# Kernel optimization log

Measured on AMD Instinct MI355X. Metric: run time of the kernel, lower is better.

Reference implementation:

```python
import jax, jax.numpy as jnp
import numpy as np

# Stickbreaking attention (IBM ModuleFormer style) as in the torch module:
#   logits = q @ k^T / sqrt(head_dim)  (causal)
#   z = sigmoid(logits), log_beta = logsigmoid(-logits), both causally masked
#   re_cum_log_beta = einsum('bhij,jk->bhik', log_beta, tril(ones(S,S)))
#     -> re[i,k] = sum_{k <= j <= i} log_beta[i, j]   (full tril incl. diagonal,
#        exactly as written in the source: cum_weight = torch.tril(torch.ones(L,L)))
#   weights = z * exp(re_cum_log_beta);  out = weights @ v
# Note: the torch code applies the causal mask by adding -inf; the only finite,
# NaN-free expression of that math (matching ModuleFormer's masked_fill) is to
# zero out masked entries of z and log_beta before the triangular matmul.

B, H, S, D = 2, 16, 1024, 64


def setup_inputs() -> dict:
    key = jax.random.key(0)
    kq, kk, kv = jax.random.split(key, 3)
    q = jax.random.normal(kq, (B, H, S, D), dtype=jnp.float32)
    k = jax.random.normal(kk, (B, H, S, D), dtype=jnp.float32)
    v = jax.random.normal(kv, (B, H, S, D), dtype=jnp.float32)
    return {"q": q, "k": k, "v": v}


def reference(q, k, v):
    head_dim = q.shape[-1]
    scaling = 1.0 / np.sqrt(head_dim).astype(np.float32)
    # [B,H,S,S] attention logits
    logits = jnp.einsum("bhqd,bhkd->bhqk", q, k) * scaling
    seq = logits.shape[-1]
    causal = jnp.tril(jnp.ones((seq, seq), dtype=logits.dtype))  # 1 where j<=i
    z = jax.nn.sigmoid(logits) * causal
    log_beta = jax.nn.log_sigmoid(-logits) * causal
    cum_weight = jnp.tril(jnp.ones((seq, seq), dtype=logits.dtype))
    # re[i,k] = sum_{j>=k} log_beta[i,j] (log_beta already 0 for j>i)
    re_cum_log_beta = jnp.einsum("bhij,jk->bhik", log_beta, cum_weight)
    weights = z * jnp.exp(re_cum_log_beta)
    return jnp.einsum("bhqk,bhkd->bhqd", weights, v)
```

## Files before the change

kernel.cpp:

```cpp
#include <hip/hip_runtime.h>
#include <hip/hip_bf16.h>
#include <math.h>


typedef __attribute__((ext_vector_type(8))) short short8;
typedef __attribute__((ext_vector_type(4))) short short4v;
typedef __attribute__((ext_vector_type(4))) float f32x4;

#define PITCH 72

__device__ inline short bf16r(float x) {
    __hip_bfloat16 h = __float2bfloat16(x);
    return *(short*)&h;
}
__device__ inline float bf16f(short s) {
    union { unsigned u; float f; } c;
    c.u = ((unsigned)(unsigned short)s) << 16;
    return c.f;
}
__device__ inline void tsplit(float x, short &hi, short &lo) {
    union { float f; unsigned u; } c; c.f = x;
    hi = (short)(c.u >> 16);
    union { unsigned u; float f; } h; h.u = c.u & 0xFFFF0000u;
    union { float f; unsigned u; } r; r.f = x - h.f;
    lo = (short)(r.u >> 16);
}

__device__ inline void lds_barrier() {
    __builtin_amdgcn_sched_barrier(0);
    asm volatile("s_waitcnt lgkmcnt(0)" ::: "memory");
    __builtin_amdgcn_s_barrier();
    __builtin_amdgcn_sched_barrier(0);
}

__global__ __launch_bounds__(256, 2) void stickbreak_mfma(
    const float* __restrict__ Qg, const float* __restrict__ Kg,
    const float* __restrict__ Vg, float* __restrict__ Og)
{
    __shared__ __align__(16) short Kh[2][64 * PITCH];
    __shared__ __align__(16) short Kl[2][64 * PITCH];
    __shared__ __align__(16) short Vt[2][64 * PITCH];
    __shared__ __align__(16) short Ws[64 * PITCH];

    const int t = threadIdx.x;
    const int n = blockIdx.x;
    const int bh = (n & 7) + 8 * (n >> 7);
    const int qr = (n >> 3) & 15;
    const int qt = (n >> 8) ? (15 - qr) : qr;

    const size_t hbase = (size_t)bh * 1024 * 64;
    const float* qp = Qg + hbase + (size_t)qt * 64 * 64;
    const float* kp = Kg + hbase;
    const float* vp = Vg + hbase;
    float*       op = Og + hbase + (size_t)qt * 64 * 64;

    const int lane = t & 63;
    const int wv   = t >> 6;
    const int l16  = lane & 15;
    const int q4   = lane >> 4;

    const int srow = t >> 2;
    const int scol = (t & 3) << 4;
    const int vj   = (t & 15) << 2;
    const int vd   = (t >> 4) << 2;

    short8 qfh[2], qfl[2];
    {
        const float* qrow = qp + (16 * wv + l16) * 64;
        #pragma unroll
        for (int ks = 0; ks < 2; ++ks) {
            const int base = 32 * ks + 8 * q4;
            const float4 f0 = *(const float4*)(qrow + base);
            const float4 f1 = *(const float4*)(qrow + base + 4);
            float a[8] = {f0.x, f0.y, f0.z, f0.w, f1.x, f1.y, f1.z, f1.w};
            #pragma unroll
            for (int j = 0; j < 8; ++j) {
                short hi, lo;
                tsplit(a[j], hi, lo);
                qfh[ks][j] = hi;
                qfl[ks][j] = lo;
            }
        }
    }

    f32x4 Oacc[4];
    #pragma unroll
    for (int i = 0; i < 4; ++i) Oacc[i] = (f32x4){0.f, 0.f, 0.f, 0.f};
    float Prow = 1.f;

    float4 kreg[4], vreg[4];

    auto prefetch_tile = [&](int tt) {
        const float* ksrc = kp + (size_t)tt * 4096 + srow * 64 + scol;
        const float* vsrc = vp + (size_t)tt * 4096;
        #pragma unroll
        for (int i = 0; i < 4; ++i) kreg[i] = *(const float4*)(ksrc + 4 * i);
        #pragma unroll
        for (int r = 0; r < 4; ++r) vreg[r] = *(const float4*)(vsrc + (vj + r) * 64 + vd);
    };

    auto stage_tile = [&](int nb) {
        short8 h0, h1, l0, l1;
        #pragma unroll
        for (int i = 0; i < 4; ++i) {
            float a[4] = {kreg[i].x, kreg[i].y, kreg[i].z, kreg[i].w};
            #pragma unroll
            for (int j = 0; j < 4; ++j) {
                short hi, lo;
                tsplit(a[j], hi, lo);
                const int idx = 4 * i + j;
                if (idx < 8) { h0[idx] = hi; l0[idx] = lo; }
                else         { h1[idx - 8] = hi; l1[idx - 8] = lo; }
            }
        }
        *(short8*)&Kh[nb][srow * PITCH + scol]     = h0;
        *(short8*)&Kh[nb][srow * PITCH + scol + 8] = h1;
        *(short8*)&Kl[nb][srow * PITCH + scol]     = l0;
        *(short8*)&Kl[nb][srow * PITCH + scol + 8] = l1;
        #pragma unroll
        for (int x = 0; x < 4; ++x) {
            float rr[4] = { x == 0 ? vreg[0].x : x == 1 ? vreg[0].y : x == 2 ? vreg[0].z : vreg[0].w,
                            x == 0 ? vreg[1].x : x == 1 ? vreg[1].y : x == 2 ? vreg[1].z : vreg[1].w,
                            x == 0 ? vreg[2].x : x == 1 ? vreg[2].y : x == 2 ? vreg[2].z : vreg[2].w,
                            x == 0 ? vreg[3].x : x == 1 ? vreg[3].y : x == 2 ? vreg[3].z : vreg[3].w };
            short4v w4;
            #pragma unroll
            for (int r = 0; r < 4; ++r) w4[r] = bf16r(rr[r]);
            *(short4v*)&Vt[nb][(vd + x) * PITCH + vj] = w4;
        }
    };

    prefetch_tile(qt);
    stage_tile(0);
    if (qt > 0) prefetch_tile(qt - 1);
    lds_barrier();

    for (int kt = qt; kt >= 0; --kt) {
        const int cur = (qt - kt) & 1;

        f32x4 Sacc[4];
        #pragma unroll
        for (int i = 0; i < 4; ++i) Sacc[i] = (f32x4){0.f, 0.f, 0.f, 0.f};
        #pragma unroll
        for (int ks = 0; ks < 2; ++ks) {
            #pragma unroll
            for (int nt = 0; nt < 4; ++nt) {
                const short8 ah = *(const short8*)&Kh[cur][(16 * nt + l16) * PITCH + 32 * ks + 8 * q4];
                const short8 al = *(const short8*)&Kl[cur][(16 * nt + l16) * PITCH + 32 * ks + 8 * q4];
                Sacc[nt] = __builtin_amdgcn_mfma_f32_16x16x32_bf16(ah, qfh[ks], Sacc[nt], 0, 0, 0);
                Sacc[nt] = __builtin_amdgcn_mfma_f32_16x16x32_bf16(al, qfh[ks], Sacc[nt], 0, 0, 0);
                Sacc[nt] = __builtin_amdgcn_mfma_f32_16x16x32_bf16(ah, qfl[ks], Sacc[nt], 0, 0, 0);
            }
        }

        const bool diag = (kt == qt);
        const int irow = 16 * wv + l16;
        const float C = 0.180336880f;
        float zp[4][4];
        float sR[4];
        #pragma unroll
        for (int nt = 0; nt < 4; ++nt) {
            float b[4], zz[4];
            #pragma unroll
            for (int reg = 0; reg < 4; ++reg) {
                float l2 = Sacc[nt][reg] * C;
                if (diag && (16 * nt + 4 * q4 + reg > irow)) l2 = -1e30f;
                l2 = fminf(l2, 80.f);
                const float e  = __builtin_amdgcn_exp2f(l2);
                const float bb = __builtin_amdgcn_rcpf(1.f + e);
                b[reg] = bb;
                zz[reg] = e * bb;
            }
            const float p3 = b[3];
            const float p2 = b[2] * p3;
            const float p1 = b[1] * p2;
            const float p0 = b[0] * p1;
            zp[nt][0] = zz[0] * p0;
            zp[nt][1] = zz[1] * p1;
            zp[nt][2] = zz[2] * p2;
            zp[nt][3] = zz[3] * p3;
            sR[nt] = p0;
        }
        float ex4[4], Tn[4];
        #pragma unroll
        for (int nt = 0; nt < 4; ++nt) {
            float g = sR[nt];
            float u = __shfl_down(g, 16, 64); if (q4 < 3) g *= u;
            u = __shfl_down(g, 32, 64);       if (q4 < 2) g *= u;
            const float x = __shfl_down(g, 16, 64);
            ex4[nt] = (q4 == 3) ? 1.f : x;
            Tn[nt]  = __shfl(g, l16, 64);
        }
        const float TSa[4] = { Tn[1] * Tn[2] * Tn[3], Tn[2] * Tn[3], Tn[3], 1.f };
        #pragma unroll
        for (int nt = 0; nt < 4; ++nt) {
            const float cross = ex4[nt] * TSa[nt] * Prow;
            short4v w4;
            #pragma unroll
            for (int reg = 0; reg < 4; ++reg)
                w4[reg] = bf16r(zp[nt][reg] * cross);
            *(short4v*)&Ws[irow * PITCH + 16 * nt + 4 * q4] = w4;
        }
        Prow *= TSa[0] * Tn[0];

        #pragma unroll
        for (int ks = 0; ks < 2; ++ks) {
            const short8 wa = *(const short8*)&Ws[(16 * wv + l16) * PITCH + 32 * ks + 8 * q4];
            #pragma unroll
            for (int dt = 0; dt < 4; ++dt) {
                const short8 vb = *(const short8*)&Vt[cur][(16 * dt + l16) * PITCH + 32 * ks + 8 * q4];
                Oacc[dt] = __builtin_amdgcn_mfma_f32_16x16x32_bf16(wa, vb, Oacc[dt], 0, 0, 0);
            }
        }

        if (kt > 0) {
            stage_tile(cur ^ 1);
            if (kt > 1) prefetch_tile(kt - 2);
            lds_barrier();
        }
    }

    #pragma unroll
    for (int dt = 0; dt < 4; ++dt)
        #pragma unroll
        for (int r = 0; r < 4; ++r)
            op[(16 * wv + 4 * q4 + r) * 64 + 16 * dt + l16] = Oacc[dt][r];
}

extern "C" void kernel_launch(void* const* d_in, const int* in_sizes, int n_in,
                              void* d_out, int out_size, void* d_ws, size_t ws_size,
                              hipStream_t stream) {
    const float* q = (const float*)d_in[0];
    const float* k = (const float*)d_in[1];
    const float* v = (const float*)d_in[2];
    float* out = (float*)d_out;
    stickbreak_mfma<<<dim3(512), dim3(256), 0, stream>>>(q, k, v, out);
}
```

Before: 96.73 us.

## Permute K tile rows so score accumulators feed PV MFMA directly from registers

K rows are written to shared memory in a permuted order, so the S=K·Q MFMA output lands in registers in exactly the layout the W·V MFMA needs as its A operand. This removes the Ws shared-memory round trip (a store, a reload and the implied ordering) and rewrites the stick-breaking prefix products around the new column ordering, with fewer shuffles. The cost is more intricate index math for the causal mask and the cumulative products, which raises the risk of subtle ordering errors.

```diff
diff --git a/kernel.cpp b/kernel.cpp
--- a/kernel.cpp
+++ b/kernel.cpp
@@ -40,7 +40,6 @@
     __shared__ __align__(16) short Kh[2][64 * PITCH];
     __shared__ __align__(16) short Kl[2][64 * PITCH];
     __shared__ __align__(16) short Vt[2][64 * PITCH];
-    __shared__ __align__(16) short Ws[64 * PITCH];
 
     const int t = threadIdx.x;
     const int n = blockIdx.x;
@@ -61,6 +60,8 @@
 
     const int srow = t >> 2;
     const int scol = (t & 3) << 4;
+    const int kprm = (((srow >> 2) & 1) << 5) | (((srow >> 5) & 1) << 4)
+                   | (((srow >> 3) & 3) << 2) | (srow & 3);
     const int vj   = (t & 15) << 2;
     const int vd   = (t >> 4) << 2;
 
@@ -113,10 +114,10 @@
                 else         { h1[idx - 8] = hi; l1[idx - 8] = lo; }
             }
         }
-        *(short8*)&Kh[nb][srow * PITCH + scol]     = h0;
-        *(short8*)&Kh[nb][srow * PITCH + scol + 8] = h1;
-        *(short8*)&Kl[nb][srow * PITCH + scol]     = l0;
-        *(short8*)&Kl[nb][srow * PITCH + scol + 8] = l1;
+        *(short8*)&Kh[nb][kprm * PITCH + scol]     = h0;
+        *(short8*)&Kh[nb][kprm * PITCH + scol + 8] = h1;
+        *(short8*)&Kl[nb][kprm * PITCH + scol]     = l0;
+        *(short8*)&Kl[nb][kprm * PITCH + scol + 8] = l1;
         #pragma unroll
         for (int x = 0; x < 4; ++x) {
             float rr[4] = { x == 0 ? vreg[0].x : x == 1 ? vreg[0].y : x == 2 ? vreg[0].z : vreg[0].w,
@@ -164,53 +165,56 @@
             #pragma unroll
             for (int reg = 0; reg < 4; ++reg) {
                 float l2 = Sacc[nt][reg] * C;
-                if (diag && (16 * nt + 4 * q4 + reg > irow)) l2 = -1e30f;
+                const int j = 32 * (nt & 1) + 8 * q4 + 4 * (nt >> 1) + reg;
+                if (diag && (j > irow)) l2 = -1e30f;
                 l2 = fminf(l2, 80.f);
                 const float e  = __builtin_amdgcn_exp2f(l2);
                 const float bb = __builtin_amdgcn_rcpf(1.f + e);
                 b[reg] = bb;
                 zz[reg] = e * bb;
             }
-            const float p3 = b[3];
-            const float p2 = b[2] * p3;
-            const float p1 = b[1] * p2;
-            const float p0 = b[0] * p1;
-            zp[nt][0] = zz[0] * p0;
-            zp[nt][1] = zz[1] * p1;
-            zp[nt][2] = zz[2] * p2;
-            zp[nt][3] = zz[3] * p3;
-            sR[nt] = p0;
-        }
-        float ex4[4], Tn[4];
-        #pragma unroll
-        for (int nt = 0; nt < 4; ++nt) {
-            float g = sR[nt];
-            float u = __shfl_down(g, 16, 64); if (q4 < 3) g *= u;
-            u = __shfl_down(g, 32, 64);       if (q4 < 2) g *= u;
-            const float x = __shfl_down(g, 16, 64);
-            ex4[nt] = (q4 == 3) ? 1.f : x;
-            Tn[nt]  = __shfl(g, l16, 64);
-        }
-        const float TSa[4] = { Tn[1] * Tn[2] * Tn[3], Tn[2] * Tn[3], Tn[3], 1.f };
-        #pragma unroll
-        for (int nt = 0; nt < 4; ++nt) {
-            const float cross = ex4[nt] * TSa[nt] * Prow;
-            short4v w4;
-            #pragma unroll
-            for (int reg = 0; reg < 4; ++reg)
-                w4[reg] = bf16r(zp[nt][reg] * cross);
-            *(short4v*)&Ws[irow * PITCH + 16 * nt + 4 * q4] = w4;
-        }
-        Prow *= TSa[0] * Tn[0];
-
-        #pragma unroll
-        for (int ks = 0; ks < 2; ++ks) {
-            const short8 wa = *(const short8*)&Ws[(16 * wv + l16) * PITCH + 32 * ks + 8 * q4];
-            #pragma unroll
-            for (int dt = 0; dt < 4; ++dt) {
-                const short8 vb = *(const short8*)&Vt[cur][(16 * dt + l16) * PITCH + 32 * ks + 8 * q4];
-                Oacc[dt] = __builtin_amdgcn_mfma_f32_16x16x32_bf16(wa, vb, Oacc[dt], 0, 0, 0);
-            }
+            const float s3 = b[3];
+            const float s2 = b[2] * s3;
+            const float s1 = b[1] * s2;
+            const float s0 = b[0] * s1;
+            zp[nt][0] = zz[0] * s0;
+            zp[nt][1] = zz[1] * s1;
+            zp[nt][2] = zz[2] * s2;
+            zp[nt][3] = zz[3] * s3;
+            sR[nt] = s0;
+        }
+        #pragma unroll
+        for (int reg = 0; reg < 4; ++reg) { zp[0][reg] *= sR[2]; zp[1][reg] *= sR[3]; }
+        const float R0 = sR[0] * sR[2];
+        const float R1 = sR[1] * sR[3];
+        float gU = R1, gL = R0, u;
+        u = __shfl_down(gU, 16, 64); if (q4 < 3) gU *= u;
+        u = __shfl_down(gU, 32, 64); if (q4 < 2) gU *= u;
+        float exU = __shfl_down(gU, 16, 64); if (q4 == 3) exU = 1.f;
+        const float T1 = __shfl(gU, l16, 64);
+        u = __shfl_down(gL, 16, 64); if (q4 < 3) gL *= u;
+        u = __shfl_down(gL, 32, 64); if (q4 < 2) gL *= u;
+        float exL = __shfl_down(gL, 16, 64); if (q4 == 3) exL = 1.f;
+        const float T0 = __shfl(gL, l16, 64);
+        const float mulU = exU * Prow;
+        const float mulL = exL * T1 * Prow;
+        Prow *= T1 * T0;
+
+        short8 wf0, wf1;
+        #pragma unroll
+        for (int reg = 0; reg < 4; ++reg) {
+            wf0[reg]     = bf16r(zp[0][reg] * mulL);
+            wf0[4 + reg] = bf16r(zp[2][reg] * mulL);
+            wf1[reg]     = bf16r(zp[1][reg] * mulU);
+            wf1[4 + reg] = bf16r(zp[3][reg] * mulU);
+        }
+
+        #pragma unroll
+        for (int dt = 0; dt < 4; ++dt) {
+            const short8 vb0 = *(const short8*)&Vt[cur][(16 * dt + l16) * PITCH + 8 * q4];
+            Oacc[dt] = __builtin_amdgcn_mfma_f32_16x16x32_bf16(wf0, vb0, Oacc[dt], 0, 0, 0);
+            const short8 vb1 = *(const short8*)&Vt[cur][(16 * dt + l16) * PITCH + 32 + 8 * q4];
+            Oacc[dt] = __builtin_amdgcn_mfma_f32_16x16x32_bf16(wf1, vb1, Oacc[dt], 0, 0, 0);
         }
 
         if (kt > 0) {
```

Result: slower. 100.8 us (+4.2%).
